# Kernel tuning notes

Measured on AMD Instinct MI355X. Metric: run time of the kernel, lower is better.

The kernel has to match this reference:

```python
import jax, jax.numpy as jnp
import numpy as np

N, K, M, DIM = 131072, 16, 128, 64


def setup_inputs() -> dict:
    key = jax.random.key(0)
    kx, ks, ka, kb = jax.random.split(key, 4)
    return {
        "x": jax.random.normal(kx, (N, DIM), dtype=jnp.float32),
        "s": jax.random.normal(ks, (K,), dtype=jnp.float32),
        "a": jax.random.normal(ka, (K, M, DIM), dtype=jnp.float32),
        "b": jax.random.normal(kb, (K, M), dtype=jnp.float32),
    }


def reference(x, s, a, b):
    # scores[k, n, m] = x[n, :] @ a[k, m, :] + b[k, m]  (batched GEMM over k)
    scores = jnp.einsum("nd,kmd->knm", x, a) + b[:, None, :]
    # per-expert logsumexp over the m affine pieces -> [k, n]
    lse = jax.nn.logsumexp(scores, axis=-1)
    # signed sum over experts -> [n]
    return jnp.einsum("k,kn->n", s, lse)
```

## Files before the change

### kernel.cpp

```cpp
#include <hip/hip_runtime.h>
#include <hip/hip_bf16.h>

#define NROWS 131072
#define KEXP 16
#define MPC 128
#define DIMD 64

typedef float f32x4  __attribute__((ext_vector_type(4)));
typedef float f32x16 __attribute__((ext_vector_type(16)));
typedef short s16x8  __attribute__((ext_vector_type(8)));

#define L2E 1.4426950408889634f
#define LN2 0.6931471805599453f

static __device__ inline unsigned int b2u(__hip_bfloat162 h) {
    union { __hip_bfloat162 h; unsigned int u; } c;
    c.h = h;
    return c.u;
}

static __device__ inline int4 cvt8s(float4 f0, float4 f1, float sc) {
    __hip_bfloat162 p0 = __float22bfloat162_rn(make_float2(f0.x * sc, f0.y * sc));
    __hip_bfloat162 p1 = __float22bfloat162_rn(make_float2(f0.z * sc, f0.w * sc));
    __hip_bfloat162 p2 = __float22bfloat162_rn(make_float2(f1.x * sc, f1.y * sc));
    __hip_bfloat162 p3 = __float22bfloat162_rn(make_float2(f1.z * sc, f1.w * sc));
    int4 pk;
    pk.x = (int)b2u(p0); pk.y = (int)b2u(p1); pk.z = (int)b2u(p2); pk.w = (int)b2u(p3);
    return pk;
}

__global__ void prep_kernel(const float* __restrict__ a, const float* __restrict__ b,
                            short* __restrict__ abff) {
    const int u   = blockIdx.x * 256 + threadIdx.x;
    const int k   = u / 1280;
    const int rem = u - k * 1280;
    const int mt  = rem / 320;
    const int rc  = rem - mt * 320;
    const int c   = rc >> 6;
    const int ul  = rc & 63;
    int4 pk;
    if (c < 4) {
        const float* p = a + (size_t)(k * MPC + mt * 32 + (ul & 31)) * DIMD
                           + c * 16 + (ul >> 5) * 8;
        pk = cvt8s(*(const float4*)(p), *(const float4*)(p + 4), L2E);
    } else {
        pk.x = 0; pk.y = 0; pk.z = 0; pk.w = 0;
        if (ul < 32) {
            union { __hip_bfloat16 h; unsigned short us; } cv;
            cv.h = __float2bfloat16(b[k * MPC + mt * 32 + ul] * L2E);
            pk.x = (int)cv.us;
        }
    }
    *(int4*)(abff + (size_t)u * 8) = pk;
}

__global__ __launch_bounds__(256, 3)
void fused_kernel(const float* __restrict__ x, const float* __restrict__ s,
                  const short* __restrict__ abff, float* __restrict__ out) {
    const int tid  = threadIdx.x;
    const int w    = tid >> 6;
    const int l    = tid & 63;
    const int ln   = l & 31;
    const int half = l >> 5;

    const int family = blockIdx.x & 1;
    const int r0w    = (blockIdx.x >> 1) * 256 + w * 64;

    union { int4 i; s16x8 v; } Bf[2][4];
#pragma unroll
    for (int nt = 0; nt < 2; ++nt)
#pragma unroll
        for (int c = 0; c < 4; ++c) {
            const float* gp = x + (size_t)(r0w + nt * 32 + ln) * DIMD + c * 16 + half * 8;
            float4 f0 = *(const float4*)(gp);
            float4 f1 = *(const float4*)(gp + 4);
            Bf[nt][c].i = cvt8s(f0, f1, 1.0f);
        }

    union { int4 i; s16x8 v; } Bones;
    Bones.i.x = (half == 0) ? 0x3F80 : 0;
    Bones.i.y = 0; Bones.i.z = 0; Bones.i.w = 0;

    float racc0 = 0.f, racc1 = 0.f;

    for (int k = 0; k < 8; ++k) {
        const int   kf   = family * 8 + k;
        const float sk2  = s[kf] * LN2;
        const short* base = abff + (size_t)kf * 10240 + l * 8;

        float esum0 = 0.f, esum1 = 0.f;

#pragma unroll
        for (int mt = 0; mt < 4; ++mt) {
            s16x8 Af[5];
#pragma unroll
            for (int c = 0; c < 5; ++c)
                Af[c] = *(const s16x8*)(base + (mt * 5 + c) * 512);

            f32x16 accA = {}, accB = {};
#pragma unroll
            for (int c = 0; c < 4; ++c) {
                accA = __builtin_amdgcn_mfma_f32_32x32x16_bf16(Af[c], Bf[0][c].v, accA, 0, 0, 0);
                accB = __builtin_amdgcn_mfma_f32_32x32x16_bf16(Af[c], Bf[1][c].v, accB, 0, 0, 0);
            }
            accA = __builtin_amdgcn_mfma_f32_32x32x16_bf16(Af[4], Bones.v, accA, 0, 0, 0);
            accB = __builtin_amdgcn_mfma_f32_32x32x16_bf16(Af[4], Bones.v, accB, 0, 0, 0);

            {
                float a0 = 0.f, a1 = 0.f, a2 = 0.f, a3 = 0.f;
                float b0 = 0.f, b1 = 0.f, b2 = 0.f, b3 = 0.f;
#pragma unroll
                for (int r = 0; r < 4; ++r) {
                    a0 += __builtin_amdgcn_exp2f(accA[4 * r + 0]);
                    a1 += __builtin_amdgcn_exp2f(accA[4 * r + 1]);
                    a2 += __builtin_amdgcn_exp2f(accA[4 * r + 2]);
                    a3 += __builtin_amdgcn_exp2f(accA[4 * r + 3]);
                    b0 += __builtin_amdgcn_exp2f(accB[4 * r + 0]);
                    b1 += __builtin_amdgcn_exp2f(accB[4 * r + 1]);
                    b2 += __builtin_amdgcn_exp2f(accB[4 * r + 2]);
                    b3 += __builtin_amdgcn_exp2f(accB[4 * r + 3]);
                }
                esum0 += (a0 + a1) + (a2 + a3);
                esum1 += (b0 + b1) + (b2 + b3);
            }
        }

        float tot0 = esum0 + __shfl_xor(esum0, 32);
        float tot1 = esum1 + __shfl_xor(esum1, 32);
        racc0 = fmaf(sk2, __log2f(tot0), racc0);
        racc1 = fmaf(sk2, __log2f(tot1), racc1);
    }

    atomicAdd(&out[r0w + half * 32 + ln], half ? racc1 : racc0);
}

extern "C" void kernel_launch(void* const* d_in, const int* in_sizes, int n_in,
                              void* d_out, int out_size, void* d_ws, size_t ws_size,
                              hipStream_t stream) {
    const float* x = (const float*)d_in[0];
    const float* s = (const float*)d_in[1];
    const float* a = (const float*)d_in[2];
    const float* b = (const float*)d_in[3];
    float* out = (float*)d_out;

    short* abff = (short*)d_ws;

    hipMemsetAsync(d_out, 0, (size_t)NROWS * sizeof(float), stream);
    prep_kernel<<<80, 256, 0, stream>>>(a, b, abff);
    fused_kernel<<<NROWS / 128, 256, 0, stream>>>(x, s, abff, out);
}
```

Baseline: 127.6 us.

## Keep expert weights in registers per wave and stage x tiles in LDS

Drops the separate prep kernel. Each wave now owns one expert, converts that expert's 128x64 weights and bias to bf16 in registers, and reuses them across 256 rows of x. The x tile is converted once per block into shared memory and shared by four waves (four experts), and the grid grows to four expert families. The aim is to remove repeated global/L2 reads of the packed weights and the extra launch. The cost is more x reloads across blocks (each x row read four times), many more atomicAdds (one per expert per row), and higher register pressure from 16 held A fragments.

```diff
diff --git a/kernel.cpp b/kernel.cpp
--- a/kernel.cpp
+++ b/kernel.cpp
@@ -29,109 +29,92 @@
     return pk;
 }
 
-__global__ void prep_kernel(const float* __restrict__ a, const float* __restrict__ b,
-                            short* __restrict__ abff) {
-    const int u   = blockIdx.x * 256 + threadIdx.x;
-    const int k   = u / 1280;
-    const int rem = u - k * 1280;
-    const int mt  = rem / 320;
-    const int rc  = rem - mt * 320;
-    const int c   = rc >> 6;
-    const int ul  = rc & 63;
-    int4 pk;
-    if (c < 4) {
-        const float* p = a + (size_t)(k * MPC + mt * 32 + (ul & 31)) * DIMD
-                           + c * 16 + (ul >> 5) * 8;
-        pk = cvt8s(*(const float4*)(p), *(const float4*)(p + 4), L2E);
-    } else {
-        pk.x = 0; pk.y = 0; pk.z = 0; pk.w = 0;
-        if (ul < 32) {
-            union { __hip_bfloat16 h; unsigned short us; } cv;
-            cv.h = __float2bfloat16(b[k * MPC + mt * 32 + ul] * L2E);
-            pk.x = (int)cv.us;
-        }
-    }
-    *(int4*)(abff + (size_t)u * 8) = pk;
-}
-
 __global__ __launch_bounds__(256, 3)
 void fused_kernel(const float* __restrict__ x, const float* __restrict__ s,
-                  const short* __restrict__ abff, float* __restrict__ out) {
+                  const float* __restrict__ a, const float* __restrict__ b,
+                  float* __restrict__ out) {
+    __shared__ int4 xbuf[2048];
+
     const int tid  = threadIdx.x;
     const int w    = tid >> 6;
     const int l    = tid & 63;
     const int ln   = l & 31;
     const int half = l >> 5;
 
-    const int family = blockIdx.x & 1;
-    const int r0w    = (blockIdx.x >> 1) * 256 + w * 64;
+    const int family = blockIdx.x & 3;
+    const int r0     = (blockIdx.x >> 2) * 256;
+    const int k      = family * 4 + w;
 
-    union { int4 i; s16x8 v; } Bf[2][4];
+    union { int4 i; s16x8 v; } Afr[16];
 #pragma unroll
-    for (int nt = 0; nt < 2; ++nt)
+    for (int mt = 0; mt < 4; ++mt)
 #pragma unroll
         for (int c = 0; c < 4; ++c) {
-            const float* gp = x + (size_t)(r0w + nt * 32 + ln) * DIMD + c * 16 + half * 8;
-            float4 f0 = *(const float4*)(gp);
-            float4 f1 = *(const float4*)(gp + 4);
-            Bf[nt][c].i = cvt8s(f0, f1, 1.0f);
+            const float* p = a + (size_t)(k * MPC + mt * 32 + ln) * DIMD + c * 16 + half * 8;
+            Afr[mt * 4 + c].i = cvt8s(*(const float4*)(p), *(const float4*)(p + 4), L2E);
         }
+
+    union { int4 i; s16x8 v; } A5[4];
+#pragma unroll
+    for (int mt = 0; mt < 4; ++mt) {
+        A5[mt].i.x = 0; A5[mt].i.y = 0; A5[mt].i.z = 0; A5[mt].i.w = 0;
+        if (half == 0) {
+            union { __hip_bfloat16 h; unsigned short us; } cv;
+            cv.h = __float2bfloat16(b[k * MPC + mt * 32 + ln] * L2E);
+            A5[mt].i.x = (int)cv.us;
+        }
+    }
 
     union { int4 i; s16x8 v; } Bones;
     Bones.i.x = (half == 0) ? 0x3F80 : 0;
     Bones.i.y = 0; Bones.i.z = 0; Bones.i.w = 0;
 
-    float racc0 = 0.f, racc1 = 0.f;
-
-    for (int k = 0; k < 8; ++k) {
-        const int   kf   = family * 8 + k;
-        const float sk2  = s[kf] * LN2;
-        const short* base = abff + (size_t)kf * 10240 + l * 8;
-
-        float esum0 = 0.f, esum1 = 0.f;
+    const float sk2 = s[k] * LN2;
 
 #pragma unroll
+    for (int i = 0; i < 8; ++i) {
+        const int u     = i * 256 + tid;
+        const int chunk = u >> 6;
+        const int nt    = chunk >> 2;
+        const int c     = chunk & 3;
+        const int ll    = u & 63;
+        const float* gp = x + (size_t)(r0 + nt * 32 + (ll & 31)) * DIMD
+                            + c * 16 + (ll >> 5) * 8;
+        xbuf[u] = cvt8s(*(const float4*)(gp), *(const float4*)(gp + 4), 1.0f);
+    }
+    __syncthreads();
+
+#pragma unroll 2
+    for (int nt = 0; nt < 8; ++nt) {
+        s16x8 Bx[4];
+#pragma unroll
+        for (int c = 0; c < 4; ++c)
+            Bx[c] = *(const s16x8*)&xbuf[(nt * 4 + c) * 64 + l];
+
+        float esum = 0.f;
+#pragma unroll
         for (int mt = 0; mt < 4; ++mt) {
-            s16x8 Af[5];
+            f32x16 acc = {};
 #pragma unroll
-            for (int c = 0; c < 5; ++c)
-                Af[c] = *(const s16x8*)(base + (mt * 5 + c) * 512);
+            for (int c = 0; c < 4; ++c)
+                acc = __builtin_amdgcn_mfma_f32_32x32x16_bf16(Afr[mt * 4 + c].v, Bx[c], acc, 0, 0, 0);
+            acc = __builtin_amdgcn_mfma_f32_32x32x16_bf16(A5[mt].v, Bones.v, acc, 0, 0, 0);
 
-            f32x16 accA = {}, accB = {};
+            float s0 = 0.f, s1 = 0.f, s2 = 0.f, s3 = 0.f;
 #pragma unroll
-            for (int c = 0; c < 4; ++c) {
-                accA = __builtin_amdgcn_mfma_f32_32x32x16_bf16(Af[c], Bf[0][c].v, accA, 0, 0, 0);
-                accB = __builtin_amdgcn_mfma_f32_32x32x16_bf16(Af[c], Bf[1][c].v, accB, 0, 0, 0);
+            for (int r = 0; r < 4; ++r) {
+                s0 += __builtin_amdgcn_exp2f(acc[4 * r + 0]);
+                s1 += __builtin_amdgcn_exp2f(acc[4 * r + 1]);
+                s2 += __builtin_amdgcn_exp2f(acc[4 * r + 2]);
+                s3 += __builtin_amdgcn_exp2f(acc[4 * r + 3]);
             }
-            accA = __builtin_amdgcn_mfma_f32_32x32x16_bf16(Af[4], Bones.v, accA, 0, 0, 0);
-            accB = __builtin_amdgcn_mfma_f32_32x32x16_bf16(Af[4], Bones.v, accB, 0, 0, 0);
-
-            {
-                float a0 = 0.f, a1 = 0.f, a2 = 0.f, a3 = 0.f;
-                float b0 = 0.f, b1 = 0.f, b2 = 0.f, b3 = 0.f;
-#pragma unroll
-                for (int r = 0; r < 4; ++r) {
-                    a0 += __builtin_amdgcn_exp2f(accA[4 * r + 0]);
-                    a1 += __builtin_amdgcn_exp2f(accA[4 * r + 1]);
-                    a2 += __builtin_amdgcn_exp2f(accA[4 * r + 2]);
-                    a3 += __builtin_amdgcn_exp2f(accA[4 * r + 3]);
-                    b0 += __builtin_amdgcn_exp2f(accB[4 * r + 0]);
-                    b1 += __builtin_amdgcn_exp2f(accB[4 * r + 1]);
-                    b2 += __builtin_amdgcn_exp2f(accB[4 * r + 2]);
-                    b3 += __builtin_amdgcn_exp2f(accB[4 * r + 3]);
-                }
-                esum0 += (a0 + a1) + (a2 + a3);
-                esum1 += (b0 + b1) + (b2 + b3);
-            }
+            esum += (s0 + s1) + (s2 + s3);
         }
 
-        float tot0 = esum0 + __shfl_xor(esum0, 32);
-        float tot1 = esum1 + __shfl_xor(esum1, 32);
-        racc0 = fmaf(sk2, __log2f(tot0), racc0);
-        racc1 = fmaf(sk2, __log2f(tot1), racc1);
+        float tot = esum + __shfl_xor(esum, 32);
+        if (half == 0)
+            atomicAdd(&out[r0 + nt * 32 + ln], sk2 * __log2f(tot));
     }
-
-    atomicAdd(&out[r0w + half * 32 + ln], half ? racc1 : racc0);
 }
 
 extern "C" void kernel_launch(void* const* d_in, const int* in_sizes, int n_in,
@@ -143,9 +126,6 @@
     const float* b = (const float*)d_in[3];
     float* out = (float*)d_out;
 
-    short* abff = (short*)d_ws;
-
     hipMemsetAsync(d_out, 0, (size_t)NROWS * sizeof(float), stream);
-    prep_kernel<<<80, 256, 0, stream>>>(a, b, abff);
-    fused_kernel<<<NROWS / 128, 256, 0, stream>>>(x, s, abff, out);
+    fused_kernel<<<(NROWS / 256) * 4, 256, 0, stream>>>(x, s, a, b, out);
 }
```

Result: slower. 135.3 us (+6.0%).
